# Kernel tuning notes

Measured on AMD Instinct MI355X. Metric: run time of the kernel, lower is better.

The kernel has to match this reference:

```python
import math
import jax, jax.numpy as jnp
import numpy as np

N_NODES = 50000
N_EDGES = 800000
FEAT = 64          # m * p == p * n == 64
P = 8              # product_size
M = FEAT // P      # 8


def setup_inputs() -> dict:
    key = jax.random.key(0)
    k1, k2, k3, k4 = jax.random.split(key, 4)
    src_feat = jax.random.normal(k1, (N_NODES, FEAT), dtype=jnp.float32)
    dst_feat = jax.random.normal(k2, (N_NODES, FEAT), dtype=jnp.float32)
    edge_src = jax.random.randint(k3, (N_EDGES,), 0, N_NODES, dtype=jnp.int32)
    edge_dst = jax.random.randint(k4, (N_EDGES,), 0, N_NODES, dtype=jnp.int32)
    return {"src_feat": src_feat, "dst_feat": dst_feat,
            "edge_src": edge_src, "edge_dst": edge_dst}


def reference(src_feat, dst_feat, edge_src, edge_dst):
    # src.view(..., -1, P) ; dst.view(..., P, -1)
    src = src_feat.reshape(N_NODES, M, P)          # [N, m, p]
    dst = dst_feat.reshape(N_NODES, P, M)          # [N, p, n]
    # per-edge SDDMM-style batched matmul: gather endpoints, matmul
    e_src = src[edge_src]                          # [E, m, p]
    e_dst = dst[edge_dst]                          # [E, p, n]
    ft_e = jnp.einsum('eij,ejk->eik', e_src, e_dst)  # [E, m, n]
    # sum-aggregate edge features onto destination nodes
    agg = jax.ops.segment_sum(ft_e, edge_dst, num_segments=N_NODES)  # [N, m, n]
    result = agg / math.sqrt(P)
    # squeeze: flatten last two dims
    return result.reshape(N_NODES, M * M)
```

## Files before the change

kernel.cpp:

```cpp
#include <hip/hip_runtime.h>
#include <hip/hip_bf16.h>

#define N_NODES 50000
#define N_EDGES 800000
#define FEAT 64
#define RANGE 32
#define NBINS 1563
#define K1B 250
#define EPB (N_EDGES / K1B)
#define SUB 16
#define RSTRIDE 4096
#define CAPP 48
#define BSTRIDE 52
#define DUMMY N_NODES
#define CONVB 391

static __device__ __forceinline__ unsigned short f2bu(float f) {
    __hip_bfloat16 h = __float2bfloat16(f);
    return __builtin_bit_cast(unsigned short, h);
}

__global__ __launch_bounds__(1024) void conv_bin_kernel(
    const float* __restrict__ src_feat,
    unsigned short* __restrict__ src16,
    const int* __restrict__ edge_src,
    const int* __restrict__ edge_dst,
    int* __restrict__ counts,
    int* __restrict__ ent)
{
    __shared__ int h[NBINS];
    int tid = threadIdx.x;

    if (blockIdx.x < CONVB) {
        int base = (blockIdx.x * 1024 + tid) * 8;
        if (base >= (N_NODES + 1) * FEAT) return;
        uint4 o;
        if (base < N_NODES * FEAT) {
            float4 a = *(const float4*)(src_feat + base);
            float4 b = *(const float4*)(src_feat + base + 4);
            o.x = (unsigned)f2bu(a.x) | ((unsigned)f2bu(a.y) << 16);
            o.y = (unsigned)f2bu(a.z) | ((unsigned)f2bu(a.w) << 16);
            o.z = (unsigned)f2bu(b.x) | ((unsigned)f2bu(b.y) << 16);
            o.w = (unsigned)f2bu(b.z) | ((unsigned)f2bu(b.w) << 16);
        } else {
            o = make_uint4(0, 0, 0, 0);
        }
        *(uint4*)(src16 + base) = o;
        return;
    }

    int b = blockIdx.x - CONVB;
    for (int r = tid; r < NBINS; r += 1024) h[r] = 0;
    __syncthreads();

    if (tid < EPB / 4) {
        int e = b * EPB + tid * 4;
        int4 s4 = *(const int4*)(edge_src + e);
        int4 d4 = *(const int4*)(edge_dst + e);
        int r0 = d4.x >> 5, r1 = d4.y >> 5, r2 = d4.z >> 5, r3 = d4.w >> 5;
        int p0 = atomicAdd(&h[r0], 1);
        int p1 = atomicAdd(&h[r1], 1);
        int p2 = atomicAdd(&h[r2], 1);
        int p3 = atomicAdd(&h[r3], 1);
        if (p0 < SUB) ent[r0 * RSTRIDE + b * SUB + p0] = ((d4.x & 31) << 16) | s4.x;
        if (p1 < SUB) ent[r1 * RSTRIDE + b * SUB + p1] = ((d4.y & 31) << 16) | s4.y;
        if (p2 < SUB) ent[r2 * RSTRIDE + b * SUB + p2] = ((d4.z & 31) << 16) | s4.z;
        if (p3 < SUB) ent[r3 * RSTRIDE + b * SUB + p3] = ((d4.w & 31) << 16) | s4.w;
    }
    __syncthreads();

    for (int r = tid; r < NBINS; r += 1024) {
        int c = h[r];
        counts[b * NBINS + r] = (c > SUB) ? SUB : c;
    }
}

#define RDIDX(ID, Q)                                                          \
    _Pragma("unroll")                                                         \
    for (int m_ = 0; m_ < 4; ++m_) {                                          \
        int raw_ = bucket_w[(wave * 4 + m_) * BSTRIDE + (Q) * 4 + sub];       \
        ID[m_] = ((Q) < rows4[m_]) ? raw_ : DUMMY;                            \
    }
#define GLOAD(L, ID)                                                          \
    _Pragma("unroll")                                                         \
    for (int m_ = 0; m_ < 4; ++m_)                                            \
        L[m_] = *(const uint2*)(src16 + (size_t)ID[m_] * FEAT + fc * 4);
#define ACCUM(L)                                                              \
    _Pragma("unroll")                                                         \
    for (int m_ = 0; m_ < 4; ++m_) {                                          \
        acc[m_][0] += __uint_as_float(L[m_].x << 16);                         \
        acc[m_][1] += __uint_as_float(L[m_].x & 0xFFFF0000u);                 \
        acc[m_][2] += __uint_as_float(L[m_].y << 16);                         \
        acc[m_][3] += __uint_as_float(L[m_].y & 0xFFFF0000u);                 \
    }

__global__ __launch_bounds__(512, 6) void sort_gather_mm_kernel(
    const unsigned short* __restrict__ src16,
    const float* __restrict__ dst_feat,
    const int* __restrict__ counts,
    const int* __restrict__ ent,
    float* __restrict__ out)
{
    __shared__ int bucket_w[RANGE * BSTRIDE];
    __shared__ int cnt_s[256];
    __shared__ int c[RANGE];

    int r = blockIdx.x;
    int tid = threadIdx.x;
    int wave = tid >> 6;
    int lane = tid & 63;

    const int* er = ent + (size_t)r * RSTRIDE;
    int ew[8];
    #pragma unroll
    for (int k = 0; k < 8; ++k)
        ew[k] = er[tid + k * 512];

    if (tid < 256) cnt_s[tid] = (tid < K1B) ? counts[tid * NBINS + r] : 0;
    if (tid < RANGE) c[tid] = 0;

    float Bv[4];
    #pragma unroll
    for (int m = 0; m < 4; ++m) {
        int n = r * RANGE + wave * 4 + m;
        Bv[m] = (n < N_NODES) ? dst_feat[n * FEAT + lane] : 0.f;
    }
    __syncthreads();

    #pragma unroll
    for (int k = 0; k < 8; ++k) {
        int g = tid + k * 512;
        int bb = g >> 4;
        int s  = g & 15;
        if (s < cnt_s[bb]) {
            int p = ew[k];
            int dl = p >> 16;
            int pos = atomicAdd(&c[dl], 1);
            if (pos < CAPP) bucket_w[dl * BSTRIDE + pos] = p & 0xFFFF;
        }
    }
    __syncthreads();

    if (tid < RANGE) {
        int cc = c[tid]; if (cc > CAPP) cc = CAPP;
        while (cc & 3) bucket_w[tid * BSTRIDE + cc++] = DUMMY;
        c[tid] = cc >> 2;
    }
    __syncthreads();

    int sub = lane >> 4;
    int fc  = lane & 15;
    int rows4[4], qmax = 0;
    #pragma unroll
    for (int m = 0; m < 4; ++m) {
        rows4[m] = c[wave * 4 + m];
        qmax = (rows4[m] > qmax) ? rows4[m] : qmax;
    }

    float acc[4][4] = {{0.f,0.f,0.f,0.f},{0.f,0.f,0.f,0.f},
                       {0.f,0.f,0.f,0.f},{0.f,0.f,0.f,0.f}};
    {
        int idA[4], idB[4];
        uint2 LA[4], LB[4];
        if (qmax > 0) { RDIDX(idA, 0); GLOAD(LA, idA); }
        int q = 0;
        while (q < qmax) {
            int qn = q + 1;
            if (qn < qmax) { RDIDX(idB, qn); GLOAD(LB, idB); }
            ACCUM(LA);
            q = qn;
            if (q >= qmax) break;
            qn = q + 1;
            if (qn < qmax) { RDIDX(idA, qn); GLOAD(LA, idA); }
            ACCUM(LB);
            q = qn;
        }
    }

    #pragma unroll
    for (int m = 0; m < 4; ++m) {
        #pragma unroll
        for (int u = 0; u < 4; ++u) {
            acc[m][u] += __shfl_xor(acc[m][u], 16, 64);
            acc[m][u] += __shfl_xor(acc[m][u], 32, 64);
        }
    }

    int i = lane >> 3;
    int j = lane & 7;
    #pragma unroll
    for (int m = 0; m < 4; ++m) {
        int n = r * RANGE + wave * 4 + m;
        if (n >= N_NODES) break;
        float res = 0.0f;
        #pragma unroll
        for (int p = 0; p < 8; ++p) {
            float s_ip = __shfl(acc[m][p & 3], 2 * i + (p >> 2), 64);
            float b_pj = __shfl(Bv[m], p * 8 + j, 64);
            res += s_ip * b_pj;
        }
        out[n * FEAT + lane] = res * 0.35355339059327373f;
    }
}

extern "C" void kernel_launch(void* const* d_in, const int* in_sizes, int n_in,
                              void* d_out, int out_size, void* d_ws, size_t ws_size,
                              hipStream_t stream) {
    const float* src_feat = (const float*)d_in[0];
    const float* dst_feat = (const float*)d_in[1];
    const int* edge_src = (const int*)d_in[2];
    const int* edge_dst = (const int*)d_in[3];
    float* out = (float*)d_out;

    char* w = (char*)d_ws;
    int* counts = (int*)w;                        w += 1563008;
    int* ent = (int*)w;                           w += (size_t)NBINS * RSTRIDE * 4;
    unsigned short* src16 = (unsigned short*)w;

    conv_bin_kernel<<<CONVB + K1B, 1024, 0, stream>>>(
        src_feat, src16, edge_src, edge_dst, counts, ent);

    sort_gather_mm_kernel<<<NBINS, 512, 0, stream>>>(
        src16, dst_feat, counts, ent, out);
}
```

Baseline: 115.7 us.

## Replace two-level binned sort with per-node global atomic cursor scatter

Drops the shared-memory histogram binning and the per-block sub-bucket layout. Edges are now scattered straight into fixed-capacity per-destination-node slots using global atomic cursors, after a zeroing pass, and the gather kernel loads those slots directly without a local sort phase. This removes the large sparse ent buffer reads and the in-block atomic re-bucketing. In exchange it adds a third kernel launch and 800k global atomics spread over 50k addresses, and the scatter writes ent2 non-coalesced.

```diff
diff --git a/kernel.cpp b/kernel.cpp
--- a/kernel.cpp
+++ b/kernel.cpp
@@ -6,31 +6,24 @@
 #define FEAT 64
 #define RANGE 32
 #define NBINS 1563
-#define K1B 250
-#define EPB (N_EDGES / K1B)
-#define SUB 16
-#define RSTRIDE 4096
 #define CAPP 48
-#define BSTRIDE 52
+#define NCUR 50016
 #define DUMMY N_NODES
 #define CONVB 391
+#define ZEROB 13
+
 
 static __device__ __forceinline__ unsigned short f2bu(float f) {
     __hip_bfloat16 h = __float2bfloat16(f);
     return __builtin_bit_cast(unsigned short, h);
 }
 
-__global__ __launch_bounds__(1024) void conv_bin_kernel(
+__global__ __launch_bounds__(1024) void conv_zero_kernel(
     const float* __restrict__ src_feat,
     unsigned short* __restrict__ src16,
-    const int* __restrict__ edge_src,
-    const int* __restrict__ edge_dst,
-    int* __restrict__ counts,
-    int* __restrict__ ent)
+    int* __restrict__ cursor)
 {
-    __shared__ int h[NBINS];
     int tid = threadIdx.x;
-
     if (blockIdx.x < CONVB) {
         int base = (blockIdx.x * 1024 + tid) * 8;
         if (base >= (N_NODES + 1) * FEAT) return;
@@ -48,38 +41,35 @@
         *(uint4*)(src16 + base) = o;
         return;
     }
+    int idx = (blockIdx.x - CONVB) * 1024 + tid;
+    if (idx < NCUR / 4) ((int4*)cursor)[idx] = make_int4(0, 0, 0, 0);
+}
 
-    int b = blockIdx.x - CONVB;
-    for (int r = tid; r < NBINS; r += 1024) h[r] = 0;
-    __syncthreads();
-
-    if (tid < EPB / 4) {
-        int e = b * EPB + tid * 4;
-        int4 s4 = *(const int4*)(edge_src + e);
-        int4 d4 = *(const int4*)(edge_dst + e);
-        int r0 = d4.x >> 5, r1 = d4.y >> 5, r2 = d4.z >> 5, r3 = d4.w >> 5;
-        int p0 = atomicAdd(&h[r0], 1);
-        int p1 = atomicAdd(&h[r1], 1);
-        int p2 = atomicAdd(&h[r2], 1);
-        int p3 = atomicAdd(&h[r3], 1);
-        if (p0 < SUB) ent[r0 * RSTRIDE + b * SUB + p0] = ((d4.x & 31) << 16) | s4.x;
-        if (p1 < SUB) ent[r1 * RSTRIDE + b * SUB + p1] = ((d4.y & 31) << 16) | s4.y;
-        if (p2 < SUB) ent[r2 * RSTRIDE + b * SUB + p2] = ((d4.z & 31) << 16) | s4.z;
-        if (p3 < SUB) ent[r3 * RSTRIDE + b * SUB + p3] = ((d4.w & 31) << 16) | s4.w;
-    }
-    __syncthreads();
-
-    for (int r = tid; r < NBINS; r += 1024) {
-        int c = h[r];
-        counts[b * NBINS + r] = (c > SUB) ? SUB : c;
-    }
+__global__ __launch_bounds__(1024) void scatter_kernel(
+    const int* __restrict__ edge_src,
+    const int* __restrict__ edge_dst,
+    int* __restrict__ cursor,
+    int* __restrict__ ent2)
+{
+    int t = blockIdx.x * 1024 + threadIdx.x;
+    if (t >= N_EDGES / 4) return;
+    int4 s4 = ((const int4*)edge_src)[t];
+    int4 d4 = ((const int4*)edge_dst)[t];
+    int p0 = atomicAdd(&cursor[d4.x], 1);
+    int p1 = atomicAdd(&cursor[d4.y], 1);
+    int p2 = atomicAdd(&cursor[d4.z], 1);
+    int p3 = atomicAdd(&cursor[d4.w], 1);
+    if (p0 < CAPP) ent2[(size_t)d4.x * CAPP + p0] = s4.x;
+    if (p1 < CAPP) ent2[(size_t)d4.y * CAPP + p1] = s4.y;
+    if (p2 < CAPP) ent2[(size_t)d4.z * CAPP + p2] = s4.z;
+    if (p3 < CAPP) ent2[(size_t)d4.w * CAPP + p3] = s4.w;
 }
 
 #define RDIDX(ID, Q)                                                          \
     _Pragma("unroll")                                                         \
     for (int m_ = 0; m_ < 4; ++m_) {                                          \
-        int raw_ = bucket_w[(wave * 4 + m_) * BSTRIDE + (Q) * 4 + sub];       \
-        ID[m_] = ((Q) < rows4[m_]) ? raw_ : DUMMY;                            \
+        int raw_ = ids[(wave * 4 + m_) * CAPP + (Q) * 4 + sub];               \
+        ID[m_] = ((Q) * 4 + sub < dg[m_]) ? raw_ : DUMMY;                     \
     }
 #define GLOAD(L, ID)                                                          \
     _Pragma("unroll")                                                         \
@@ -94,30 +84,27 @@
         acc[m_][3] += __uint_as_float(L[m_].y & 0xFFFF0000u);                 \
     }
 
-__global__ __launch_bounds__(512, 6) void sort_gather_mm_kernel(
+__global__ __launch_bounds__(512, 6) void gather_mm_kernel(
     const unsigned short* __restrict__ src16,
     const float* __restrict__ dst_feat,
-    const int* __restrict__ counts,
-    const int* __restrict__ ent,
+    const int* __restrict__ cursor,
+    const int* __restrict__ ent2,
     float* __restrict__ out)
 {
-    __shared__ int bucket_w[RANGE * BSTRIDE];
-    __shared__ int cnt_s[256];
-    __shared__ int c[RANGE];
+    __shared__ int ids[RANGE * CAPP];
+    __shared__ int degs_s[RANGE];
 
     int r = blockIdx.x;
     int tid = threadIdx.x;
     int wave = tid >> 6;
     int lane = tid & 63;
 
-    const int* er = ent + (size_t)r * RSTRIDE;
-    int ew[8];
-    #pragma unroll
-    for (int k = 0; k < 8; ++k)
-        ew[k] = er[tid + k * 512];
-
-    if (tid < 256) cnt_s[tid] = (tid < K1B) ? counts[tid * NBINS + r] : 0;
-    if (tid < RANGE) c[tid] = 0;
+    const int4* gsrc = (const int4*)(ent2 + (size_t)r * RANGE * CAPP);
+    if (tid < RANGE * CAPP / 4) ((int4*)ids)[tid] = gsrc[tid];
+    if (tid < RANGE) {
+        int d = cursor[r * RANGE + tid];
+        degs_s[tid] = (d > CAPP) ? CAPP : d;
+    }
 
     float Bv[4];
     #pragma unroll
@@ -127,33 +114,13 @@
     }
     __syncthreads();
 
-    #pragma unroll
-    for (int k = 0; k < 8; ++k) {
-        int g = tid + k * 512;
-        int bb = g >> 4;
-        int s  = g & 15;
-        if (s < cnt_s[bb]) {
-            int p = ew[k];
-            int dl = p >> 16;
-            int pos = atomicAdd(&c[dl], 1);
-            if (pos < CAPP) bucket_w[dl * BSTRIDE + pos] = p & 0xFFFF;
-        }
-    }
-    __syncthreads();
-
-    if (tid < RANGE) {
-        int cc = c[tid]; if (cc > CAPP) cc = CAPP;
-        while (cc & 3) bucket_w[tid * BSTRIDE + cc++] = DUMMY;
-        c[tid] = cc >> 2;
-    }
-    __syncthreads();
-
     int sub = lane >> 4;
     int fc  = lane & 15;
-    int rows4[4], qmax = 0;
+    int dg[4], rows4[4], qmax = 0;
     #pragma unroll
     for (int m = 0; m < 4; ++m) {
-        rows4[m] = c[wave * 4 + m];
+        dg[m] = degs_s[wave * 4 + m];
+        rows4[m] = (dg[m] + 3) >> 2;
         qmax = (rows4[m] > qmax) ? rows4[m] : qmax;
     }
 
@@ -213,13 +180,13 @@
     float* out = (float*)d_out;
 
     char* w = (char*)d_ws;
-    int* counts = (int*)w;                        w += 1563008;
-    int* ent = (int*)w;                           w += (size_t)NBINS * RSTRIDE * 4;
+    int* cursor = (int*)w;                        w += (size_t)NCUR * 4;
+    int* ent2 = (int*)w;                          w += (size_t)NCUR * CAPP * 4;
     unsigned short* src16 = (unsigned short*)w;
 
-    conv_bin_kernel<<<CONVB + K1B, 1024, 0, stream>>>(
-        src_feat, src16, edge_src, edge_dst, counts, ent);
+    conv_zero_kernel<<<CONVB + ZEROB, 1024, 0, stream>>>(src_feat, src16, cursor);
 
-    sort_gather_mm_kernel<<<NBINS, 512, 0, stream>>>(
-        src16, dst_feat, counts, ent, out);
+    scatter_kernel<<<196, 1024, 0, stream>>>(edge_src, edge_dst, cursor, ent2);
+
+    gather_mm_kernel<<<NBINS, 512, 0, stream>>>(src16, dst_feat, cursor, ent2, out);
 }
```

Result: slower. 138.6 us (+19.8%).
